# Performance work log

Hardware: AMD Instinct MI355X
Metric: run time of the kernel (lower is better)

## Reference

```python
import jax, jax.numpy as jnp
import numpy as np

N = 10000          # num nodes
E = 160000         # num edges (avg degree 16)
F = 128            # num_features
S = 4              # num_species
RAD = 8            # radial_embedding_dim
RO = 16            # readout_mlp_irreps = 16x0e
EPS = 0.17677669529663687  # epsilon = 1/sqrt(avg_degree)
ACT_NORM = 1.679177        # normalize_function(silu): 1/sqrt(E[silu(x)^2]), x~N(0,1)


def nsilu(x):
    return jax.nn.silu(x) * ACT_NORM


def setup_inputs() -> dict:
    key = jax.random.key(0)
    ks = jax.random.split(key, 24)
    d = {}
    d["vectors"] = jax.random.normal(ks[0], (E, 3), jnp.float32)
    d["node_scalars"] = jax.random.normal(ks[1], (N, F), jnp.float32)
    d["node_vectors"] = jax.random.normal(ks[2], (N, F, 3), jnp.float32)
    d["radial_embeddings"] = jax.random.normal(ks[3], (E, RAD), jnp.float32)
    # linear_up (irrep-wise linear on 0e and 1o)
    d["W_up_s"] = jax.random.normal(ks[4], (F, F), jnp.float32)
    d["W_up_v"] = jax.random.normal(ks[5], (F, F), jnp.float32)
    # radial MLP [RAD,64,64,64,weight_dim=4F]
    d["W_mlp1"] = jax.random.normal(ks[6], (RAD, 64), jnp.float32) / np.sqrt(RAD)
    d["b_mlp1"] = jnp.zeros((64,), jnp.float32)
    d["W_mlp2"] = jax.random.normal(ks[7], (64, 64), jnp.float32) / np.sqrt(64.0)
    d["b_mlp2"] = jnp.zeros((64,), jnp.float32)
    d["W_mlp3"] = jax.random.normal(ks[8], (64, 64), jnp.float32) / np.sqrt(64.0)
    d["b_mlp3"] = jnp.zeros((64,), jnp.float32)
    d["W_mlp4"] = jax.random.normal(ks[9], (64, 4 * F), jnp.float32) / np.sqrt(64.0)
    d["b_mlp4"] = jnp.zeros((4 * F,), jnp.float32)
    # linear_down: TP out (2F x 0e + 2F x 1o) -> F x (0e+1o)
    d["W_down_s"] = jax.random.normal(ks[10], (2 * F, F), jnp.float32)
    d["W_down_v"] = jax.random.normal(ks[11], (2 * F, F), jnp.float32)
    # species-indexed skip linear (output is hidden_out = 0e only, since last=True)
    d["Wz_s"] = jax.random.normal(ks[12], (S, F, F), jnp.float32)
    # symmetric contraction weights: 5 invariant basis terms per channel per species
    d["W_sc"] = jax.random.normal(ks[13], (S, 5, F), jnp.float32)
    d["W_post"] = jax.random.normal(ks[14], (F, F), jnp.float32)
    d["W_ro1"] = jax.random.normal(ks[15], (F, RO), jnp.float32)
    d["W_ro2"] = jax.random.normal(ks[16], (RO, 1), jnp.float32)
    d["senders"] = jax.random.randint(ks[17], (E,), 0, N)
    d["receivers"] = jax.random.randint(ks[18], (E,), 0, N)
    d["num_species_counts"] = jnp.full((S,), N // S, dtype=jnp.int32)
    d["num_nodes"] = N
    return d


def reference(vectors, node_scalars, node_vectors, radial_embeddings,
              W_up_s, W_up_v,
              W_mlp1, b_mlp1, W_mlp2, b_mlp2, W_mlp3, b_mlp3, W_mlp4, b_mlp4,
              W_down_s, W_down_v, Wz_s, W_sc, W_post, W_ro1, W_ro2,
              senders, receivers, num_species_counts, num_nodes):
    # spherical harmonics (max_ell=1): Y0 = 1, Y1 = unit edge vector
    rnorm = jnp.linalg.norm(vectors, axis=-1, keepdims=True)
    Y1 = vectors / (rnorm + 1e-12)                      # [E,3]

    # species index per node from counts
    i = jnp.repeat(jnp.arange(S), num_species_counts, total_repeat_length=num_nodes)

    # self connection (species-indexed linear on input scalars; hidden_out = 0e)
    self_conn = jnp.einsum('nf,nfg->ng', node_scalars, Wz_s[i]) / np.sqrt(F)

    # linear_up (irrep-wise)
    s = node_scalars @ W_up_s / np.sqrt(F)              # [N,F]
    v = jnp.einsum('nfc,fg->ngc', node_vectors, W_up_v) / np.sqrt(F)  # [N,F,3]

    # radial MLP -> per-edge channelwise TP weights, 4 paths x F channels
    h = nsilu(radial_embeddings @ W_mlp1 + b_mlp1)
    h = nsilu(h @ W_mlp2 + b_mlp2)
    h = nsilu(h @ W_mlp3 + b_mlp3)
    mix = (h @ W_mlp4 + b_mlp4).reshape(-1, 4, F)       # [E,4,F]

    # channelwise tensor product: gather sender feats, combine with sph
    sg = s[senders]                                     # [E,F]
    vg = v[senders]                                     # [E,F,3]
    m_s0 = mix[:, 0] * sg                               # 0e x 0e -> 0e
    m_s3 = mix[:, 3] * (jnp.einsum('efc,ec->ef', vg, Y1) / np.sqrt(3.0))  # 1o x 1o -> 0e
    m_v1 = mix[:, 1][..., None] * sg[..., None] * Y1[:, None, :]          # 0e x 1o -> 1o
    m_v2 = mix[:, 2][..., None] * vg                                      # 1o x 0e -> 1o
    msg_s = jnp.concatenate([m_s0, m_s3], axis=-1)      # [E,2F]
    msg_v = jnp.concatenate([m_v1, m_v2], axis=1)       # [E,2F,3]

    # scatter to receivers
    agg_s = jax.ops.segment_sum(msg_s, receivers, num_segments=num_nodes) * EPS
    agg_v = jax.ops.segment_sum(msg_v, receivers, num_segments=num_nodes) * EPS

    # linear_down: 2F -> F per irrep
    s2 = agg_s @ W_down_s / np.sqrt(2 * F)              # [N,F]
    v2 = jnp.einsum('nfc,fg->ngc', agg_v, W_down_v) / np.sqrt(2 * F)  # [N,F,3]

    # symmetric contraction (correlation<=3, output 0e): per-species weighted
    # invariant basis {s, s^2, |v|^2, s^3, s|v|^2} per channel
    vv = jnp.sum(v2 * v2, axis=-1)                      # [N,F]
    basis = jnp.stack([s2, s2 * s2, vv, s2 * s2 * s2, s2 * vv], axis=1)  # [N,5,F]
    sc = jnp.sum(W_sc[i] * basis, axis=1)               # [N,F]

    feats = sc @ W_post / np.sqrt(F) + self_conn        # [N,F]

    # readout (last=True): linear -> scalar activation -> linear
    hr = nsilu(feats @ W_ro1 / np.sqrt(F))              # [N,16]
    node_outputs = hr @ W_ro2 / np.sqrt(RO)             # [N,1]
    return (node_outputs, feats)
```

## Files before the change

kernel.cpp:

```cpp
#include <hip/hip_runtime.h>
#include <hip/hip_bf16.h>
#include <math.h>

#define N_NODES 10000
#define N_EDGES 160000
#define F 128
#define TE 128
#define HS 72

typedef _Float16 v8h __attribute__((ext_vector_type(8)));
typedef _Float16 v4h __attribute__((ext_vector_type(4)));
typedef float    v4f __attribute__((ext_vector_type(4)));

__device__ __forceinline__ float nsilu(float x) {
    return 1.679177f * (x / (1.0f + expf(-x)));
}

__device__ __forceinline__ void fma4(float4& a, float s, const float4& b) {
    a.x = fmaf(s, b.x, a.x); a.y = fmaf(s, b.y, a.y);
    a.z = fmaf(s, b.z, a.z); a.w = fmaf(s, b.w, a.w);
}

__device__ __forceinline__ int species_of(int n, const int* __restrict__ counts) {
    int c0 = counts[0];
    int c01 = c0 + counts[1];
    int c012 = c01 + counts[2];
    return (n >= c0) + (n >= c01) + (n >= c012);
}

__global__ __launch_bounds__(256) void k_setup(
    const int* __restrict__ receivers, int* __restrict__ deg,
    const float* __restrict__ W2, const float* __restrict__ W3,
    const float* __restrict__ W4, const float* __restrict__ b4,
    const float* __restrict__ Wup_s, const float* __restrict__ Wup_v,
    const float* __restrict__ Wz, const float* __restrict__ Wds,
    const float* __restrict__ Wdv, const float* __restrict__ Wpost,
    _Float16* __restrict__ W2t, _Float16* __restrict__ W3t,
    _Float16* __restrict__ W4t, float* __restrict__ b4p,
    _Float16* __restrict__ Wup_s_t, _Float16* __restrict__ Wup_v_t,
    _Float16* __restrict__ Wz_t, _Float16* __restrict__ Wds_t,
    _Float16* __restrict__ Wdv_t, _Float16* __restrict__ Wpost_t,
    const float* __restrict__ ns, const float* __restrict__ nv,
    _Float16* __restrict__ ns16, _Float16* __restrict__ nv16)
{
    int gidx = blockIdx.x * 256 + threadIdx.x;
    if (gidx < N_EDGES) {
        atomicAdd(&deg[receivers[gidx]], 1);
        return;
    }
    int idx = gidx - N_EDGES;
    if (idx < 221696) {
        if (idx < 4096) {
            int u = idx >> 6, k = idx & 63;
            W2t[idx] = (_Float16)W2[k * 64 + u];
        } else if (idx < 8192) {
            int j = idx - 4096;
            int u = j >> 6, k = j & 63;
            W3t[j] = (_Float16)W3[k * 64 + u];
        } else if (idx < 40960) {
            int j = idx - 8192;
            int gn = j >> 6, k = j & 63;
            int go = (gn & 3) * 128 + (gn >> 2);
            W4t[j] = (_Float16)W4[k * 512 + go];
        } else if (idx < 41472) {
            int j = idx - 40960;
            int go = (j & 3) * 128 + (j >> 2);
            b4p[j] = b4[go];
        } else if (idx < 57856) {
            int j = idx - 41472;
            int g = j >> 7, f = j & 127;
            Wup_s_t[j] = (_Float16)Wup_s[f * 128 + g];
        } else if (idx < 74240) {
            int j = idx - 57856;
            int g = j >> 7, f = j & 127;
            Wup_v_t[j] = (_Float16)Wup_v[f * 128 + g];
        } else if (idx < 139776) {
            int j = idx - 74240;
            int s = j >> 14, r = j & 16383;
            int g = r >> 7, f = r & 127;
            Wz_t[j] = (_Float16)Wz[s * 16384 + f * 128 + g];
        } else if (idx < 172544) {
            int j = idx - 139776;
            int g = j >> 8, k = j & 255;
            Wds_t[j] = (_Float16)Wds[k * 128 + g];
        } else if (idx < 205312) {
            int j = idx - 172544;
            int g = j >> 8, k = j & 255;
            Wdv_t[j] = (_Float16)Wdv[k * 128 + g];
        } else {
            int j = idx - 205312;
            int g = j >> 7, f = j & 127;
            Wpost_t[j] = (_Float16)Wpost[f * 128 + g];
        }
        return;
    }
    int j = idx - 221696;
    if (j < N_NODES * F) {
        ns16[j] = (_Float16)ns[j];
    } else if (j < 4 * N_NODES * F) {
        int j2 = j - N_NODES * F;
        int row = j2 >> 7, f = j2 & 127;
        int n = row / 3, c = row - n * 3;
        nv16[j2] = (_Float16)nv[((size_t)n * F + f) * 3 + c];
    }
}

__global__ __launch_bounds__(1024) void k_scan(const int* __restrict__ deg,
                                               int* __restrict__ offs,
                                               int* __restrict__ cursor) {
    __shared__ int sums[1024];
    const int t = threadIdx.x;
    const int CH = 10;
    int base = t * CH;
    int local[CH];
    int s = 0;
    #pragma unroll
    for (int j = 0; j < CH; ++j) {
        int v = (base + j < N_NODES) ? deg[base + j] : 0;
        local[j] = s;
        s += v;
    }
    sums[t] = s;
    __syncthreads();
    for (int off = 1; off < 1024; off <<= 1) {
        int v = (t >= off) ? sums[t - off] : 0;
        __syncthreads();
        sums[t] += v;
        __syncthreads();
    }
    int carry = (t == 0) ? 0 : sums[t - 1];
    #pragma unroll
    for (int j = 0; j < CH; ++j) {
        int idx = base + j;
        if (idx < N_NODES) {
            int o = carry + local[j];
            offs[idx] = o;
            cursor[idx] = o;
        }
    }
    if (t == 1023) offs[N_NODES] = sums[1023];
}

__global__ __launch_bounds__(256) void k_fill(const int* __restrict__ receivers,
                                              const int* __restrict__ senders,
                                              const float* __restrict__ vectors,
                                              const float* __restrict__ radial,
                                              int* __restrict__ cursor,
                                              float4* __restrict__ yq,
                                              float4* __restrict__ re_csr) {
    int e = blockIdx.x * 256 + threadIdx.x;
    if (e < N_EDGES) {
        int pos = atomicAdd(&cursor[receivers[e]], 1);
        float vx = vectors[e * 3 + 0];
        float vy = vectors[e * 3 + 1];
        float vz = vectors[e * 3 + 2];
        float inv = 1.0f / (sqrtf(vx * vx + vy * vy + vz * vz) + 1e-12f);
        float4 y;
        y.x = vx * inv; y.y = vy * inv; y.z = vz * inv;
        y.w = __int_as_float(senders[e]);
        yq[pos] = y;
        const float4* rp = (const float4*)(radial + (size_t)e * 8);
        re_csr[pos * 2]     = rp[0];
        re_csr[pos * 2 + 1] = rp[1];
    }
}

template <int K, typename OT>
__device__ __forceinline__ void gemm_tile(
    const _Float16* __restrict__ A, const _Float16* __restrict__ Bg,
    OT* __restrict__ out, int M, int row0, float scale,
    _Float16* Bl, const int* __restrict__ counts, int sp)
{
    const int t = threadIdx.x;
    constexpr int KP = K + 8;
    __syncthreads();
    for (int idx = t; idx < 128 * (K / 8); idx += 256) {
        int g = idx / (K / 8), kk = (idx % (K / 8)) * 8;
        *(v8h*)(Bl + g * KP + kk) = *(const v8h*)(Bg + g * K + kk);
    }
    __syncthreads();

    const int lane = t & 63;
    const int w = t >> 6;
    const int c = lane & 15;
    const int q = lane >> 4;

    v4f acc[2][8];
    #pragma unroll
    for (int mi = 0; mi < 2; ++mi)
        #pragma unroll
        for (int nt = 0; nt < 8; ++nt)
            acc[mi][nt] = (v4f){0.f, 0.f, 0.f, 0.f};

    for (int ch = 0; ch < K / 32; ++ch) {
        v8h a[2];
        #pragma unroll
        for (int mi = 0; mi < 2; ++mi) {
            int r = row0 + (2 * w + mi) * 16 + c;
            r = min(r, M - 1);
            a[mi] = *(const v8h*)(A + (size_t)r * K + ch * 32 + q * 8);
        }
        #pragma unroll
        for (int nt = 0; nt < 8; ++nt) {
            v8h b = *(const v8h*)(Bl + (nt * 16 + c) * KP + ch * 32 + q * 8);
            acc[0][nt] = __builtin_amdgcn_mfma_f32_16x16x32_f16(a[0], b, acc[0][nt], 0, 0, 0);
            acc[1][nt] = __builtin_amdgcn_mfma_f32_16x16x32_f16(a[1], b, acc[1][nt], 0, 0, 0);
        }
    }
    #pragma unroll
    for (int mi = 0; mi < 2; ++mi) {
        #pragma unroll
        for (int r = 0; r < 4; ++r) {
            int row = row0 + (2 * w + mi) * 16 + q * 4 + r;
            bool ok = row < M;
            if (ok && sp >= 0) ok = (species_of(row, counts) == sp);
            if (ok) {
                OT* op = out + (size_t)row * 128;
                #pragma unroll
                for (int nt = 0; nt < 8; ++nt)
                    op[nt * 16 + c] = (OT)(acc[mi][nt][r] * scale);
            }
        }
    }
}

__global__ __launch_bounds__(256) void k_gemm_up(
    const _Float16* __restrict__ ns16, const _Float16* __restrict__ nv16,
    const _Float16* __restrict__ Wup_s_t, const _Float16* __restrict__ Wup_v_t,
    const _Float16* __restrict__ Wz_t, const int* __restrict__ counts,
    _Float16* __restrict__ s16, _Float16* __restrict__ v16,
    float* __restrict__ selfc)
{
    __shared__ _Float16 Bl[128 * 136];
    const int row0 = blockIdx.x * 128;
    const float isf = 0.08838834764831845f;
    if (blockIdx.y == 0) {
        if (row0 >= N_NODES) return;
        gemm_tile<128, _Float16>(ns16, Wup_s_t, s16, N_NODES, row0, isf, Bl, counts, -1);
    } else if (blockIdx.y == 1) {
        gemm_tile<128, _Float16>(nv16, Wup_v_t, v16, 3 * N_NODES, row0, isf, Bl, counts, -1);
    } else {
        if (row0 >= N_NODES) return;
        int sp0 = species_of(row0, counts);
        int sp1 = species_of(min(row0 + 127, N_NODES - 1), counts);
        for (int sp = sp0; sp <= sp1; ++sp)
            gemm_tile<128, float>(ns16, Wz_t + (size_t)sp * 16384, selfc,
                                  N_NODES, row0, isf, Bl, counts, sp);
    }
}

__global__ __launch_bounds__(256) void k_gemm_down(
    const _Float16* __restrict__ agg_s16, const _Float16* __restrict__ agg_v16,
    const _Float16* __restrict__ Wds_t, const _Float16* __restrict__ Wdv_t,
    const int* __restrict__ counts,
    float* __restrict__ s2, float* __restrict__ v2)
{
    __shared__ _Float16 Bl[128 * 264];
    const int row0 = blockIdx.x * 128;
    if (blockIdx.y == 0) {
        if (row0 >= N_NODES) return;
        gemm_tile<256, float>(agg_s16, Wds_t, s2, N_NODES, row0, 1.0f, Bl, counts, -1);
    } else {
        gemm_tile<256, float>(agg_v16, Wdv_t, v2, 3 * N_NODES, row0, 1.0f, Bl, counts, -1);
    }
}

__device__ __forceinline__ void mfma_layer64(
    const _Float16* src, _Float16* dst,
    const _Float16* __restrict__ Wt, const float* __restrict__ b,
    int w, int q, int c)
{
    v8h B[4][2];
    float bias[4];
    #pragma unroll
    for (int nt = 0; nt < 4; ++nt) {
        B[nt][0] = *(const v8h*)(Wt + (nt * 16 + c) * 64 + q * 8);
        B[nt][1] = *(const v8h*)(Wt + (nt * 16 + c) * 64 + 32 + q * 8);
        bias[nt] = b[nt * 16 + c];
    }
    #pragma unroll
    for (int mi = 0; mi < 2; ++mi) {
        int mt = 2 * w + mi;
        v8h a0 = *(const v8h*)(src + (mt * 16 + c) * HS + q * 8);
        v8h a1 = *(const v8h*)(src + (mt * 16 + c) * HS + 32 + q * 8);
        #pragma unroll
        for (int nt = 0; nt < 4; ++nt) {
            v4f acc = {bias[nt], bias[nt], bias[nt], bias[nt]};
            acc = __builtin_amdgcn_mfma_f32_16x16x32_f16(a0, B[nt][0], acc, 0, 0, 0);
            acc = __builtin_amdgcn_mfma_f32_16x16x32_f16(a1, B[nt][1], acc, 0, 0, 0);
            #pragma unroll
            for (int r = 0; r < 4; ++r)
                dst[(mt * 16 + q * 4 + r) * HS + nt * 16 + c] = (_Float16)nsilu(acc[r]);
        }
    }
}

__global__ __launch_bounds__(256) void k_mlp(
    const float* __restrict__ re_csr,
    const float* __restrict__ W1, const float* __restrict__ b1,
    const _Float16* __restrict__ W2t, const float* __restrict__ b2,
    const _Float16* __restrict__ W3t, const float* __restrict__ b3,
    const _Float16* __restrict__ W4t, const float* __restrict__ b4p,
    _Float16* __restrict__ mix)
{
    __shared__ float sre[TE * 8];
    __shared__ _Float16 hA[TE * HS];
    __shared__ _Float16 hB[TE * HS];

    const int t = threadIdx.x;
    const int p0 = blockIdx.x * TE;

    ((float4*)sre)[t] = ((const float4*)(re_csr + (size_t)p0 * 8))[t];
    __syncthreads();

    {
        const int uslot = t & 15;
        const int egrp = t >> 4;
        const int u0 = uslot * 4;
        float4 w[8];
        #pragma unroll
        for (int k = 0; k < 8; ++k) w[k] = *(const float4*)(W1 + k * 64 + u0);
        float4 bb = *(const float4*)(b1 + u0);
        #pragma unroll
        for (int i = 0; i < 8; ++i) {
            int e = egrp + i * 16;
            const float* rp = sre + e * 8;
            float4 a = bb;
            #pragma unroll
            for (int k = 0; k < 8; ++k) fma4(a, rp[k], w[k]);
            v4h r = {(_Float16)nsilu(a.x), (_Float16)nsilu(a.y),
                     (_Float16)nsilu(a.z), (_Float16)nsilu(a.w)};
            *(v4h*)(hA + e * HS + u0) = r;
        }
    }
    __syncthreads();

    const int lane = t & 63;
    const int w = t >> 6;
    const int c = lane & 15;
    const int q = lane >> 4;

    mfma_layer64(hA, hB, W2t, b2, w, q, c);
    mfma_layer64(hB, hA, W3t, b3, w, q, c);
    __syncthreads();

    v8h B4[8][2];
    float bias4[8];
    #pragma unroll
    for (int j = 0; j < 8; ++j) {
        int g = (8 * w + j) * 16 + c;
        B4[j][0] = *(const v8h*)(W4t + g * 64 + q * 8);
        B4[j][1] = *(const v8h*)(W4t + g * 64 + 32 + q * 8);
        bias4[j] = b4p[g];
    }
    for (int mt = 0; mt < 8; ++mt) {
        v8h a0 = *(const v8h*)(hA + (mt * 16 + c) * HS + q * 8);
        v8h a1 = *(const v8h*)(hA + (mt * 16 + c) * HS + 32 + q * 8);
        size_t rowbase = (size_t)(p0 + mt * 16 + q * 4) * 512;
        #pragma unroll
        for (int j = 0; j < 8; ++j) {
            v4f acc = {bias4[j], bias4[j], bias4[j], bias4[j]};
            acc = __builtin_amdgcn_mfma_f32_16x16x32_f16(a0, B4[j][0], acc, 0, 0, 0);
            acc = __builtin_amdgcn_mfma_f32_16x16x32_f16(a1, B4[j][1], acc, 0, 0, 0);
            int gcol = (8 * w + j) * 16 + c;
            #pragma unroll
            for (int r = 0; r < 4; ++r)
                mix[rowbase + (size_t)r * 512 + gcol] = (_Float16)acc[r];
        }
    }
}

__global__ __launch_bounds__(128) void k_gather(
    const _Float16* __restrict__ mix, const float4* __restrict__ yq,
    const _Float16* __restrict__ s16, const _Float16* __restrict__ v16,
    const int* __restrict__ offs,
    _Float16* __restrict__ agg_s16, _Float16* __restrict__ agg_v16)
{
    const int n = blockIdx.x;
    const int f = threadIdx.x;
    const int beg = offs[n], end = offs[n + 1];
    const float inv_sqrt3 = 0.5773502691896258f;
    __shared__ float4 ly[32];

    float as0 = 0, as1 = 0;
    float av00 = 0, av01 = 0, av02 = 0, av10 = 0, av11 = 0, av12 = 0;

    for (int c0 = beg; c0 < end; c0 += 32) {
        int cnt = min(32, end - c0);
        __syncthreads();
        if (f < cnt) ly[f] = yq[c0 + f];
        __syncthreads();
        #pragma unroll 4
        for (int i = 0; i < cnt; ++i) {
            float4 y = ly[i];
            int snd = __float_as_int(y.w);

            union { uint2 u; _Float16 h[4]; } mu;
            mu.u = *(const uint2*)(mix + (size_t)(c0 + i) * 512 + f * 4);
            float m0 = (float)mu.h[0];
            float m1 = (float)mu.h[1];
            float m2 = (float)mu.h[2];
            float m3 = (float)mu.h[3];

            float sg = (float)s16[(size_t)snd * F + f];
            const _Float16* vb = v16 + (size_t)snd * 384;
            float vg0 = (float)vb[f];
            float vg1 = (float)vb[128 + f];
            float vg2 = (float)vb[256 + f];

            as0 += m0 * sg;
            as1 += m3 * (vg0 * y.x + vg1 * y.y + vg2 * y.z) * inv_sqrt3;
            float w1s = m1 * sg;
            av00 += w1s * y.x; av01 += w1s * y.y; av02 += w1s * y.z;
            av10 += m2 * vg0;  av11 += m2 * vg1;  av12 += m2 * vg2;
        }
    }
    const float SC = 0.011048543456039804f;
    agg_s16[(size_t)n * 256 + f]       = (_Float16)(as0 * SC);
    agg_s16[(size_t)n * 256 + 128 + f] = (_Float16)(as1 * SC);
    _Float16* av = agg_v16 + (size_t)n * 768;
    av[0 * 256 + f]       = (_Float16)(av00 * SC);
    av[0 * 256 + 128 + f] = (_Float16)(av10 * SC);
    av[1 * 256 + f]       = (_Float16)(av01 * SC);
    av[1 * 256 + 128 + f] = (_Float16)(av11 * SC);
    av[2 * 256 + f]       = (_Float16)(av02 * SC);
    av[2 * 256 + 128 + f] = (_Float16)(av12 * SC);
}

__global__ __launch_bounds__(256) void k_contract(
    const float* __restrict__ s2, const float* __restrict__ v2,
    const float* __restrict__ Wsc, const int* __restrict__ counts,
    _Float16* __restrict__ sc16)
{
    int idx = blockIdx.x * 256 + threadIdx.x;
    int n = idx >> 7, g = idx & 127;
    float s = s2[idx];
    const float* vp = v2 + (size_t)n * 384;
    float a0 = vp[g], a1 = vp[128 + g], a2 = vp[256 + g];
    float vv = a0 * a0 + a1 * a1 + a2 * a2;
    const float* w = Wsc + (size_t)species_of(n, counts) * 640;
    float sc = w[g] * s + w[128 + g] * (s * s) + w[256 + g] * vv
             + w[384 + g] * (s * s * s) + w[512 + g] * (s * vv);
    sc16[idx] = (_Float16)sc;
}

__global__ __launch_bounds__(256) void k_post(
    const _Float16* __restrict__ sc16, const _Float16* __restrict__ Wpost_t,
    const float* __restrict__ selfc,
    const float* __restrict__ Wro1, const float* __restrict__ Wro2,
    float* __restrict__ out)
{
    __shared__ _Float16 Bl[128 * 136];
    __shared__ float sfeat[128][132];
    __shared__ float shr[128][16];
    const int t = threadIdx.x;
    const int row0 = blockIdx.x * 128;
    const float isf = 0.08838834764831845f;

    for (int idx = t; idx < 128 * 16; idx += 256) {
        int g = idx >> 4, kk = (idx & 15) * 8;
        *(v8h*)(Bl + g * 136 + kk) = *(const v8h*)(Wpost_t + g * 128 + kk);
    }
    __syncthreads();

    const int lane = t & 63;
    const int w = t >> 6;
    const int c = lane & 15;
    const int q = lane >> 4;

    v4f acc[2][8];
    #pragma unroll
    for (int mi = 0; mi < 2; ++mi)
        #pragma unroll
        for (int nt = 0; nt < 8; ++nt)
            acc[mi][nt] = (v4f){0.f, 0.f, 0.f, 0.f};

    for (int ch = 0; ch < 4; ++ch) {
        v8h a[2];
        #pragma unroll
        for (int mi = 0; mi < 2; ++mi) {
            int r = row0 + (2 * w + mi) * 16 + c;
            r = min(r, N_NODES - 1);
            a[mi] = *(const v8h*)(sc16 + (size_t)r * 128 + ch * 32 + q * 8);
        }
        #pragma unroll
        for (int nt = 0; nt < 8; ++nt) {
            v8h b = *(const v8h*)(Bl + (nt * 16 + c) * 136 + ch * 32 + q * 8);
            acc[0][nt] = __builtin_amdgcn_mfma_f32_16x16x32_f16(a[0], b, acc[0][nt], 0, 0, 0);
            acc[1][nt] = __builtin_amdgcn_mfma_f32_16x16x32_f16(a[1], b, acc[1][nt], 0, 0, 0);
        }
    }
    #pragma unroll
    for (int mi = 0; mi < 2; ++mi) {
        #pragma unroll
        for (int r = 0; r < 4; ++r) {
            int row = row0 + (2 * w + mi) * 16 + q * 4 + r;
            int rl = (2 * w + mi) * 16 + q * 4 + r;
            if (row < N_NODES) {
                #pragma unroll
                for (int nt = 0; nt < 8; ++nt) {
                    int col = nt * 16 + c;
                    float feat = acc[mi][nt][r] * isf + selfc[(size_t)row * 128 + col];
                    out[N_NODES + (size_t)row * 128 + col] = feat;
                    sfeat[rl][col] = feat;
                }
            } else {
                #pragma unroll
                for (int nt = 0; nt < 8; ++nt) sfeat[rl][nt * 16 + c] = 0.f;
            }
        }
    }
    __syncthreads();

    for (int idx = t; idx < 2048; idx += 256) {
        int nd = idx >> 4, u = idx & 15;
        float a = 0;
        for (int f = 0; f < 128; f += 4) {
            float4 x = *(const float4*)&sfeat[nd][f];
            a += x.x * Wro1[(f + 0) * 16 + u] + x.y * Wro1[(f + 1) * 16 + u]
               + x.z * Wro1[(f + 2) * 16 + u] + x.w * Wro1[(f + 3) * 16 + u];
        }
        shr[nd][u] = nsilu(a * isf);
    }
    __syncthreads();

    if (t < 128 && row0 + t < N_NODES) {
        float a = 0;
        #pragma unroll
        for (int j = 0; j < 16; ++j) a += shr[t][j] * Wro2[j];
        out[row0 + t] = a * 0.25f;
    }
}


extern "C" void kernel_launch(void* const* d_in, const int* in_sizes, int n_in,
                              void* d_out, int out_size, void* d_ws, size_t ws_size,
                              hipStream_t stream) {
    const float* vectors      = (const float*)d_in[0];
    const float* node_scalars = (const float*)d_in[1];
    const float* node_vectors = (const float*)d_in[2];
    const float* radial       = (const float*)d_in[3];
    const float* W_up_s       = (const float*)d_in[4];
    const float* W_up_v       = (const float*)d_in[5];
    const float* W1 = (const float*)d_in[6];
    const float* b1 = (const float*)d_in[7];
    const float* W2 = (const float*)d_in[8];
    const float* b2 = (const float*)d_in[9];
    const float* W3 = (const float*)d_in[10];
    const float* b3 = (const float*)d_in[11];
    const float* W4 = (const float*)d_in[12];
    const float* b4 = (const float*)d_in[13];
    const float* Wds  = (const float*)d_in[14];
    const float* Wdv  = (const float*)d_in[15];
    const float* Wz   = (const float*)d_in[16];
    const float* Wsc  = (const float*)d_in[17];
    const float* Wpost= (const float*)d_in[18];
    const float* Wro1 = (const float*)d_in[19];
    const float* Wro2 = (const float*)d_in[20];
    const int* senders   = (const int*)d_in[21];
    const int* receivers = (const int*)d_in[22];
    const int* counts    = (const int*)d_in[23];
    float* out = (float*)d_out;

    const size_t NF = (size_t)N_NODES * F;

    char* base = (char*)d_ws;
    _Float16* mix = (_Float16*)base;
    float* s2   = (float*)base;
    float* v2   = s2 + NF;
    _Float16* sc16 = (_Float16*)(v2 + 3 * NF);

    char* p = base + (size_t)N_EDGES * 512 * 2;
    float4* yq     = (float4*)p;          p += (size_t)N_EDGES * 16;
    _Float16* ns16 = (_Float16*)p;        p += NF * 2;
    _Float16* nv16 = (_Float16*)p;        p += 3 * NF * 2;
    _Float16* s16  = (_Float16*)p;        p += NF * 2;
    _Float16* v16  = (_Float16*)p;        p += 3 * NF * 2;
    float* selfc   = (float*)p;           p += NF * 4;
    _Float16* agg_s16 = (_Float16*)p;     p += 2 * NF * 2;
    _Float16* agg_v16 = (_Float16*)p;     p += 6 * NF * 2;
    int* deg    = (int*)p;                p += N_NODES * 4;
    int* offs   = (int*)p;                p += (N_NODES + 1) * 4 + 12;
    int* cursor = (int*)p;                p += N_NODES * 4;
    _Float16* W2t = (_Float16*)p;         p += 4096 * 2;
    _Float16* W3t = (_Float16*)p;         p += 4096 * 2;
    _Float16* W4t = (_Float16*)p;         p += 32768 * 2;
    float* b4p    = (float*)p;            p += 512 * 4;
    _Float16* Wup_s_t = (_Float16*)p;     p += 16384 * 2;
    _Float16* Wup_v_t = (_Float16*)p;     p += 16384 * 2;
    _Float16* Wz_t    = (_Float16*)p;     p += 65536 * 2;
    _Float16* Wds_t   = (_Float16*)p;     p += 32768 * 2;
    _Float16* Wdv_t   = (_Float16*)p;     p += 32768 * 2;
    _Float16* Wpost_t = (_Float16*)p;     p += 16384 * 2;

    float4* re_csr = (float4*)agg_v16;

    hipMemsetAsync(deg, 0, N_NODES * sizeof(int), stream);

    k_setup<<<21491, 256, 0, stream>>>(
        receivers, deg, W2, W3, W4, b4, W_up_s, W_up_v, Wz, Wds, Wdv, Wpost,
        W2t, W3t, W4t, b4p, Wup_s_t, Wup_v_t, Wz_t, Wds_t, Wdv_t, Wpost_t,
        node_scalars, node_vectors, ns16, nv16);

    k_scan<<<1, 1024, 0, stream>>>(deg, offs, cursor);

    k_fill<<<(N_EDGES + 255) / 256, 256, 0, stream>>>(
        receivers, senders, vectors, radial, cursor, yq, re_csr);

    k_gemm_up<<<dim3(235, 3), 256, 0, stream>>>(
        ns16, nv16, Wup_s_t, Wup_v_t, Wz_t, counts, s16, v16, selfc);

    k_mlp<<<N_EDGES / TE, 256, 0, stream>>>(
        (const float*)re_csr, W1, b1, W2t, b2, W3t, b3, W4t, b4p, mix);

    k_gather<<<N_NODES, 128, 0, stream>>>(
        mix, yq, s16, v16, offs, agg_s16, agg_v16);

    k_gemm_down<<<dim3(235, 2), 256, 0, stream>>>(
        agg_s16, agg_v16, Wds_t, Wdv_t, counts, s2, v2);

    k_contract<<<(N_NODES * F) / 256, 256, 0, stream>>>(s2, v2, Wsc, counts, sc16);

    k_post<<<(N_NODES + 127) / 128, 256, 0, stream>>>(
        sc16, Wpost_t, selfc, Wro1, Wro2, out);
}
```

Before: 304.1 us.

## Fuse radial MLP with neighbor gather using per-segment atomic accumulation

Merges the radial MLP and the per-node gather into one kernel. The MLP output (mix) is staged in LDS instead of being written to and re-read from a large E×512 fp16 global buffer, and each edge tile's messages are reduced into fp32 node aggregates with segmented atomicAdds at receiver boundaries. The down GEMM now reads fp32 aggregates, converts them to fp16 on load and applies the scale factor there. This removes roughly 160 MB of global traffic and one launch. In exchange it adds a 40 MB memset, float atomics whose order is nondeterministic, and a serial 16-step inner loop per tile.

```diff
diff --git a/kernel.cpp b/kernel.cpp
--- a/kernel.cpp
+++ b/kernel.cpp
@@ -7,6 +7,7 @@
 #define F 128
 #define TE 128
 #define HS 72
+#define JP 516
 
 typedef _Float16 v8h __attribute__((ext_vector_type(8)));
 typedef _Float16 v4h __attribute__((ext_vector_type(4)));
@@ -147,10 +148,12 @@
                                               const float* __restrict__ radial,
                                               int* __restrict__ cursor,
                                               float4* __restrict__ yq,
-                                              float4* __restrict__ re_csr) {
+                                              float4* __restrict__ re_csr,
+                                              int* __restrict__ nidq) {
     int e = blockIdx.x * 256 + threadIdx.x;
     if (e < N_EDGES) {
-        int pos = atomicAdd(&cursor[receivers[e]], 1);
+        int rcv = receivers[e];
+        int pos = atomicAdd(&cursor[rcv], 1);
         float vx = vectors[e * 3 + 0];
         float vy = vectors[e * 3 + 1];
         float vz = vectors[e * 3 + 2];
@@ -159,15 +162,25 @@
         y.x = vx * inv; y.y = vy * inv; y.z = vz * inv;
         y.w = __int_as_float(senders[e]);
         yq[pos] = y;
+        nidq[pos] = rcv;
         const float4* rp = (const float4*)(radial + (size_t)e * 8);
         re_csr[pos * 2]     = rp[0];
         re_csr[pos * 2 + 1] = rp[1];
     }
 }
 
-template <int K, typename OT>
+__device__ __forceinline__ v8h loadA8(const _Float16* p) { return *(const v8h*)p; }
+__device__ __forceinline__ v8h loadA8(const float* p) {
+    float4 x0 = *(const float4*)p;
+    float4 x1 = *(const float4*)(p + 4);
+    v8h r = {(_Float16)x0.x, (_Float16)x0.y, (_Float16)x0.z, (_Float16)x0.w,
+             (_Float16)x1.x, (_Float16)x1.y, (_Float16)x1.z, (_Float16)x1.w};
+    return r;
+}
+
+template <int K, typename AT, typename OT>
 __device__ __forceinline__ void gemm_tile(
-    const _Float16* __restrict__ A, const _Float16* __restrict__ Bg,
+    const AT* __restrict__ A, const _Float16* __restrict__ Bg,
     OT* __restrict__ out, int M, int row0, float scale,
     _Float16* Bl, const int* __restrict__ counts, int sp)
 {
@@ -198,7 +211,7 @@
         for (int mi = 0; mi < 2; ++mi) {
             int r = row0 + (2 * w + mi) * 16 + c;
             r = min(r, M - 1);
-            a[mi] = *(const v8h*)(A + (size_t)r * K + ch * 32 + q * 8);
+            a[mi] = loadA8(A + (size_t)r * K + ch * 32 + q * 8);
         }
         #pragma unroll
         for (int nt = 0; nt < 8; ++nt) {
@@ -236,32 +249,33 @@
     const float isf = 0.08838834764831845f;
     if (blockIdx.y == 0) {
         if (row0 >= N_NODES) return;
-        gemm_tile<128, _Float16>(ns16, Wup_s_t, s16, N_NODES, row0, isf, Bl, counts, -1);
+        gemm_tile<128, _Float16, _Float16>(ns16, Wup_s_t, s16, N_NODES, row0, isf, Bl, counts, -1);
     } else if (blockIdx.y == 1) {
-        gemm_tile<128, _Float16>(nv16, Wup_v_t, v16, 3 * N_NODES, row0, isf, Bl, counts, -1);
+        gemm_tile<128, _Float16, _Float16>(nv16, Wup_v_t, v16, 3 * N_NODES, row0, isf, Bl, counts, -1);
     } else {
         if (row0 >= N_NODES) return;
         int sp0 = species_of(row0, counts);
         int sp1 = species_of(min(row0 + 127, N_NODES - 1), counts);
         for (int sp = sp0; sp <= sp1; ++sp)
-            gemm_tile<128, float>(ns16, Wz_t + (size_t)sp * 16384, selfc,
-                                  N_NODES, row0, isf, Bl, counts, sp);
+            gemm_tile<128, _Float16, float>(ns16, Wz_t + (size_t)sp * 16384, selfc,
+                                            N_NODES, row0, isf, Bl, counts, sp);
     }
 }
 
 __global__ __launch_bounds__(256) void k_gemm_down(
-    const _Float16* __restrict__ agg_s16, const _Float16* __restrict__ agg_v16,
+    const float* __restrict__ agg_s32, const float* __restrict__ agg_v32,
     const _Float16* __restrict__ Wds_t, const _Float16* __restrict__ Wdv_t,
     const int* __restrict__ counts,
     float* __restrict__ s2, float* __restrict__ v2)
 {
     __shared__ _Float16 Bl[128 * 264];
     const int row0 = blockIdx.x * 128;
+    const float SC = 0.011048543456039804f;
     if (blockIdx.y == 0) {
         if (row0 >= N_NODES) return;
-        gemm_tile<256, float>(agg_s16, Wds_t, s2, N_NODES, row0, 1.0f, Bl, counts, -1);
+        gemm_tile<256, float, float>(agg_s32, Wds_t, s2, N_NODES, row0, SC, Bl, counts, -1);
     } else {
-        gemm_tile<256, float>(agg_v16, Wdv_t, v2, 3 * N_NODES, row0, 1.0f, Bl, counts, -1);
+        gemm_tile<256, float, float>(agg_v32, Wdv_t, v2, 3 * N_NODES, row0, SC, Bl, counts, -1);
     }
 }
 
@@ -295,13 +309,15 @@
     }
 }
 
-__global__ __launch_bounds__(256) void k_mlp(
+__global__ __launch_bounds__(256) void k_mlp_gather(
     const float* __restrict__ re_csr,
     const float* __restrict__ W1, const float* __restrict__ b1,
     const _Float16* __restrict__ W2t, const float* __restrict__ b2,
     const _Float16* __restrict__ W3t, const float* __restrict__ b3,
     const _Float16* __restrict__ W4t, const float* __restrict__ b4p,
-    _Float16* __restrict__ mix)
+    const float4* __restrict__ yq, const int* __restrict__ nidq,
+    const _Float16* __restrict__ s16, const _Float16* __restrict__ v16,
+    float* __restrict__ agg_s32, float* __restrict__ agg_v32)
 {
     __shared__ float sre[TE * 8];
     __shared__ _Float16 hA[TE * HS];
@@ -335,6 +351,11 @@
     }
     __syncthreads();
 
+    float4* ly = (float4*)sre;
+    int* lnid = (int*)(sre + TE * 4);
+    if (t < TE) ly[t] = yq[p0 + t];
+    else if (t < 2 * TE) lnid[t - TE] = nidq[p0 + t - TE];
+
     const int lane = t & 63;
     const int w = t >> 6;
     const int c = lane & 15;
@@ -353,78 +374,88 @@
         B4[j][1] = *(const v8h*)(W4t + g * 64 + 32 + q * 8);
         bias4[j] = b4p[g];
     }
+
+    _Float16* stage = hB;
+    const int f = t & 127;
+    const int grp = t >> 7;
+    const float inv_sqrt3 = 0.5773502691896258f;
+
+    float a0 = 0, a1 = 0, a2 = 0, a3 = 0;
+    int cur = lnid[0];
+
     for (int mt = 0; mt < 8; ++mt) {
-        v8h a0 = *(const v8h*)(hA + (mt * 16 + c) * HS + q * 8);
-        v8h a1 = *(const v8h*)(hA + (mt * 16 + c) * HS + 32 + q * 8);
-        size_t rowbase = (size_t)(p0 + mt * 16 + q * 4) * 512;
-        #pragma unroll
-        for (int j = 0; j < 8; ++j) {
-            v4f acc = {bias4[j], bias4[j], bias4[j], bias4[j]};
-            acc = __builtin_amdgcn_mfma_f32_16x16x32_f16(a0, B4[j][0], acc, 0, 0, 0);
-            acc = __builtin_amdgcn_mfma_f32_16x16x32_f16(a1, B4[j][1], acc, 0, 0, 0);
-            int gcol = (8 * w + j) * 16 + c;
+        {
+            v8h x0 = *(const v8h*)(hA + (mt * 16 + c) * HS + q * 8);
+            v8h x1 = *(const v8h*)(hA + (mt * 16 + c) * HS + 32 + q * 8);
             #pragma unroll
-            for (int r = 0; r < 4; ++r)
-                mix[rowbase + (size_t)r * 512 + gcol] = (_Float16)acc[r];
-        }
-    }
-}
-
-__global__ __launch_bounds__(128) void k_gather(
-    const _Float16* __restrict__ mix, const float4* __restrict__ yq,
-    const _Float16* __restrict__ s16, const _Float16* __restrict__ v16,
-    const int* __restrict__ offs,
-    _Float16* __restrict__ agg_s16, _Float16* __restrict__ agg_v16)
-{
-    const int n = blockIdx.x;
-    const int f = threadIdx.x;
-    const int beg = offs[n], end = offs[n + 1];
-    const float inv_sqrt3 = 0.5773502691896258f;
-    __shared__ float4 ly[32];
-
-    float as0 = 0, as1 = 0;
-    float av00 = 0, av01 = 0, av02 = 0, av10 = 0, av11 = 0, av12 = 0;
-
-    for (int c0 = beg; c0 < end; c0 += 32) {
-        int cnt = min(32, end - c0);
+            for (int j = 0; j < 8; ++j) {
+                v4f acc = {bias4[j], bias4[j], bias4[j], bias4[j]};
+                acc = __builtin_amdgcn_mfma_f32_16x16x32_f16(x0, B4[j][0], acc, 0, 0, 0);
+                acc = __builtin_amdgcn_mfma_f32_16x16x32_f16(x1, B4[j][1], acc, 0, 0, 0);
+                int col = (8 * w + j) * 16 + c;
+                #pragma unroll
+                for (int r = 0; r < 4; ++r)
+                    stage[(q * 4 + r) * JP + col] = (_Float16)acc[r];
+            }
+        }
         __syncthreads();
-        if (f < cnt) ly[f] = yq[c0 + f];
+
+        for (int i = 0; i < 16; ++i) {
+            int pi = mt * 16 + i;
+            int n_i = lnid[pi];
+            if (n_i != cur) {
+                if (grp == 0) {
+                    atomicAdd(&agg_s32[(size_t)cur * 256 + f], a0);
+                    atomicAdd(&agg_v32[((size_t)cur * 3 + 0) * 256 + f], a1);
+                    atomicAdd(&agg_v32[((size_t)cur * 3 + 1) * 256 + f], a2);
+                    atomicAdd(&agg_v32[((size_t)cur * 3 + 2) * 256 + f], a3);
+                } else {
+                    atomicAdd(&agg_s32[(size_t)cur * 256 + 128 + f], a0);
+                    atomicAdd(&agg_v32[((size_t)cur * 3 + 0) * 256 + 128 + f], a1);
+                    atomicAdd(&agg_v32[((size_t)cur * 3 + 1) * 256 + 128 + f], a2);
+                    atomicAdd(&agg_v32[((size_t)cur * 3 + 2) * 256 + 128 + f], a3);
+                }
+                a0 = a1 = a2 = a3 = 0;
+                cur = n_i;
+            }
+            float4 y = ly[pi];
+            int snd = __float_as_int(y.w);
+            union { unsigned u; _Float16 h[2]; } mm;
+            mm.u = *(const unsigned*)(stage + i * JP + f * 4 + grp * 2);
+            float mA = (float)mm.h[0];
+            float mB = (float)mm.h[1];
+            if (grp == 0) {
+                float sg = (float)s16[(size_t)snd * F + f];
+                a0 = fmaf(mA, sg, a0);
+                float w1s = mB * sg;
+                a1 = fmaf(w1s, y.x, a1);
+                a2 = fmaf(w1s, y.y, a2);
+                a3 = fmaf(w1s, y.z, a3);
+            } else {
+                const _Float16* vb = v16 + (size_t)snd * 384;
+                float vg0 = (float)vb[f];
+                float vg1 = (float)vb[128 + f];
+                float vg2 = (float)vb[256 + f];
+                float dot = vg0 * y.x + vg1 * y.y + vg2 * y.z;
+                a0 = fmaf(mB * inv_sqrt3, dot, a0);
+                a1 = fmaf(mA, vg0, a1);
+                a2 = fmaf(mA, vg1, a2);
+                a3 = fmaf(mA, vg2, a3);
+            }
+        }
         __syncthreads();
-        #pragma unroll 4
-        for (int i = 0; i < cnt; ++i) {
-            float4 y = ly[i];
-            int snd = __float_as_int(y.w);
-
-            union { uint2 u; _Float16 h[4]; } mu;
-            mu.u = *(const uint2*)(mix + (size_t)(c0 + i) * 512 + f * 4);
-            float m0 = (float)mu.h[0];
-            float m1 = (float)mu.h[1];
-            float m2 = (float)mu.h[2];
-            float m3 = (float)mu.h[3];
-
-            float sg = (float)s16[(size_t)snd * F + f];
-            const _Float16* vb = v16 + (size_t)snd * 384;
-            float vg0 = (float)vb[f];
-            float vg1 = (float)vb[128 + f];
-            float vg2 = (float)vb[256 + f];
-
-            as0 += m0 * sg;
-            as1 += m3 * (vg0 * y.x + vg1 * y.y + vg2 * y.z) * inv_sqrt3;
-            float w1s = m1 * sg;
-            av00 += w1s * y.x; av01 += w1s * y.y; av02 += w1s * y.z;
-            av10 += m2 * vg0;  av11 += m2 * vg1;  av12 += m2 * vg2;
-        }
-    }
-    const float SC = 0.011048543456039804f;
-    agg_s16[(size_t)n * 256 + f]       = (_Float16)(as0 * SC);
-    agg_s16[(size_t)n * 256 + 128 + f] = (_Float16)(as1 * SC);
-    _Float16* av = agg_v16 + (size_t)n * 768;
-    av[0 * 256 + f]       = (_Float16)(av00 * SC);
-    av[0 * 256 + 128 + f] = (_Float16)(av10 * SC);
-    av[1 * 256 + f]       = (_Float16)(av01 * SC);
-    av[1 * 256 + 128 + f] = (_Float16)(av11 * SC);
-    av[2 * 256 + f]       = (_Float16)(av02 * SC);
-    av[2 * 256 + 128 + f] = (_Float16)(av12 * SC);
+    }
+    if (grp == 0) {
+        atomicAdd(&agg_s32[(size_t)cur * 256 + f], a0);
+        atomicAdd(&agg_v32[((size_t)cur * 3 + 0) * 256 + f], a1);
+        atomicAdd(&agg_v32[((size_t)cur * 3 + 1) * 256 + f], a2);
+        atomicAdd(&agg_v32[((size_t)cur * 3 + 2) * 256 + f], a3);
+    } else {
+        atomicAdd(&agg_s32[(size_t)cur * 256 + 128 + f], a0);
+        atomicAdd(&agg_v32[((size_t)cur * 3 + 0) * 256 + 128 + f], a1);
+        atomicAdd(&agg_v32[((size_t)cur * 3 + 1) * 256 + 128 + f], a2);
+        atomicAdd(&agg_v32[((size_t)cur * 3 + 2) * 256 + 128 + f], a3);
+    }
 }
 
 __global__ __launch_bounds__(256) void k_contract(
@@ -565,20 +596,21 @@
     const size_t NF = (size_t)N_NODES * F;
 
     char* base = (char*)d_ws;
-    _Float16* mix = (_Float16*)base;
-    float* s2   = (float*)base;
-    float* v2   = s2 + NF;
+    float* s2      = (float*)base;
+    float* v2      = s2 + NF;
     _Float16* sc16 = (_Float16*)(v2 + 3 * NF);
-
-    char* p = base + (size_t)N_EDGES * 512 * 2;
+    float4* re_csr = (float4*)(sc16 + NF);
+    int* nidq      = (int*)((char*)re_csr + (size_t)N_EDGES * 32);
+    float* agg_s32 = (float*)((char*)nidq + ((size_t)N_EDGES * 4 + 12) / 16 * 16 + 16);
+    float* agg_v32 = agg_s32 + 2 * NF;
+
+    char* p = (char*)(agg_v32 + 6 * NF);
     float4* yq     = (float4*)p;          p += (size_t)N_EDGES * 16;
     _Float16* ns16 = (_Float16*)p;        p += NF * 2;
     _Float16* nv16 = (_Float16*)p;        p += 3 * NF * 2;
     _Float16* s16  = (_Float16*)p;        p += NF * 2;
     _Float16* v16  = (_Float16*)p;        p += 3 * NF * 2;
     float* selfc   = (float*)p;           p += NF * 4;
-    _Float16* agg_s16 = (_Float16*)p;     p += 2 * NF * 2;
-    _Float16* agg_v16 = (_Float16*)p;     p += 6 * NF * 2;
     int* deg    = (int*)p;                p += N_NODES * 4;
     int* offs   = (int*)p;                p += (N_NODES + 1) * 4 + 12;
     int* cursor = (int*)p;                p += N_NODES * 4;
@@ -593,9 +625,8 @@
     _Float16* Wdv_t   = (_Float16*)p;     p += 32768 * 2;
     _Float16* Wpost_t = (_Float16*)p;     p += 16384 * 2;
 
-    float4* re_csr = (float4*)agg_v16;
-
     hipMemsetAsync(deg, 0, N_NODES * sizeof(int), stream);
+    hipMemsetAsync(agg_s32, 0, (size_t)N_NODES * 1024 * sizeof(float), stream);
 
     k_setup<<<21491, 256, 0, stream>>>(
         receivers, deg, W2, W3, W4, b4, W_up_s, W_up_v, Wz, Wds, Wdv, Wpost,
@@ -605,19 +636,17 @@
     k_scan<<<1, 1024, 0, stream>>>(deg, offs, cursor);
 
     k_fill<<<(N_EDGES + 255) / 256, 256, 0, stream>>>(
-        receivers, senders, vectors, radial, cursor, yq, re_csr);
+        receivers, senders, vectors, radial, cursor, yq, re_csr, nidq);
 
     k_gemm_up<<<dim3(235, 3), 256, 0, stream>>>(
         ns16, nv16, Wup_s_t, Wup_v_t, Wz_t, counts, s16, v16, selfc);
 
-    k_mlp<<<N_EDGES / TE, 256, 0, stream>>>(
-        (const float*)re_csr, W1, b1, W2t, b2, W3t, b3, W4t, b4p, mix);
-
-    k_gather<<<N_NODES, 128, 0, stream>>>(
-        mix, yq, s16, v16, offs, agg_s16, agg_v16);
+    k_mlp_gather<<<N_EDGES / TE, 256, 0, stream>>>(
+        (const float*)re_csr, W1, b1, W2t, b2, W3t, b3, W4t, b4p,
+        yq, nidq, s16, v16, agg_s32, agg_v32);
 
     k_gemm_down<<<dim3(235, 2), 256, 0, stream>>>(
-        agg_s16, agg_v16, Wds_t, Wdv_t, counts, s2, v2);
+        agg_s32, agg_v32, Wds_t, Wdv_t, counts, s2, v2);
 
     k_contract<<<(N_NODES * F) / 256, 256, 0, stream>>>(s2, v2, Wsc, counts, sc16);
 
```

Result: slower. 373.7 us (+22.9%).
